# Optimization experiments

Measured on AMD Instinct MI355X. Metric: run time of the kernel, lower is better.

Reference implementation:

```python
import jax, jax.numpy as jnp
import numpy as np

N, E, D, T, R, H = 100000, 500000, 128, 3, 4, 8
DK = D // H
MAXLEN = 240
L = 2


def _rte_table():
    # Replicates RelTemporalEncoding sinusoidal table (note original precedence:
    # div_term = 1 / ((10000 ** arange(0, 2d, 2)) / d / 2); large exponents overflow
    # to inf in fp32 -> div entries become 0, matching torch behaviour).
    pos = jnp.arange(MAXLEN, dtype=jnp.float32)[:, None]            # [240, 1]
    ar = jnp.arange(0.0, 2 * D, 2.0, dtype=jnp.float32)             # [D]
    div = 1.0 / (jnp.power(jnp.float32(10000.0), ar) / D / 2.0)
    ang = pos * div                                                  # [240, D]
    s = np.float32(1.0 / np.sqrt(D))
    tab = jnp.zeros((MAXLEN, 2 * D), jnp.float32)
    tab = tab.at[:, 0::2].set(jnp.sin(ang) * s)
    tab = tab.at[:, 1::2].set(jnp.cos(ang) * s)
    return tab


def _typed_linear(x, W, b, types):
    # per-row type-specific affine: small fixed loop over node types
    out = jnp.zeros((x.shape[0], W.shape[-1]), x.dtype)
    for t in range(W.shape[0]):
        m = (types == t)[:, None].astype(x.dtype)
        out = out + m * (x @ W[t] + b[t])
    return out


def _typed_mm(x, W, types):
    out = jnp.zeros((x.shape[0], W.shape[-1]), x.dtype)
    for t in range(W.shape[0]):
        out = out + (types == t)[:, None].astype(x.dtype) * (x @ W[t])
    return out


def _hgt_layer(x, node_type, src, tgt, edge_type, edge_time, rte_tab,
               Wk, bk, Wq, bq, Wv, bv, Wa, ba, rel_pri, rel_att, rel_msg,
               skip, rte_w, rte_b):
    st = node_type[src]
    tt = node_type[tgt]
    # node-level typed projections (Q uses raw target feats; K/V bias+feat part)
    Qn = _typed_linear(x, Wq, bq, node_type)
    Kn = _typed_linear(x, Wk, bk, node_type)
    Vn = _typed_linear(x, Wv, bv, node_type)
    # per-edge temporal encoding added to source features before K/V linears;
    # linearity lets us add its typed projection (no double bias)
    rte = rte_tab[edge_time] @ rte_w + rte_b                         # [E, D]
    q = Qn[tgt].reshape(-1, H, DK)
    k = (Kn[src] + _typed_mm(rte, Wk, st)).reshape(-1, H, DK)
    v = (Vn[src] + _typed_mm(rte, Wv, st)).reshape(-1, H, DK)
    k2 = jnp.zeros_like(k)
    v2 = jnp.zeros_like(v)
    for r in range(R):  # small fixed relation loop, masked per-edge
        m = (edge_type == r)[:, None, None].astype(x.dtype)
        k2 = k2 + m * jnp.einsum('ehk,hkl->ehl', k, rel_att[r])
        v2 = v2 + m * jnp.einsum('ehk,hkl->ehl', v, rel_msg[r])
    pri = rel_pri[tt, edge_type, st]                                 # [E, H]
    score = (q * k2).sum(-1) * pri / np.float32(np.sqrt(DK))         # [E, H]
    # scatter-softmax over edges grouped by target node
    mx = jax.ops.segment_max(score, tgt, num_segments=N)
    ex = jnp.exp(score - mx[tgt])
    den = jax.ops.segment_sum(ex, tgt, num_segments=N)
    att = ex / den[tgt]
    msg = (v2 * att[:, :, None]).reshape(-1, D)
    aggr = jax.ops.segment_sum(msg, tgt, num_segments=N)             # [N, D]
    h = jax.nn.gelu(aggr, approximate=False)
    trans = _typed_linear(h, Wa, ba, node_type)
    alpha = jax.nn.sigmoid(skip)[node_type][:, None]
    return alpha * trans + (1.0 - alpha) * x


def setup_inputs() -> dict:
    key = jax.random.key(0)
    ks = jax.random.split(key, 20)
    s = np.float32(1.0 / np.sqrt(D))
    return {
        'node_feature': jax.random.normal(ks[0], (N, D), jnp.float32),
        'node_type': jax.random.randint(ks[1], (N,), 0, T, jnp.int32),
        'edge_index': jax.random.randint(ks[2], (2, E), 0, N, jnp.int32),
        'edge_type': jax.random.randint(ks[3], (E,), 0, R, jnp.int32),
        'edge_time': jax.random.randint(ks[4], (E,), 0, MAXLEN, jnp.int32),
        'adapt_w': jax.random.normal(ks[5], (T, D, D), jnp.float32) * s,
        'adapt_b': jax.random.normal(ks[6], (T, D), jnp.float32) * 0.01,
        'Wk': jax.random.normal(ks[7], (L, T, D, D), jnp.float32) * s,
        'bk': jax.random.normal(ks[8], (L, T, D), jnp.float32) * 0.01,
        'Wq': jax.random.normal(ks[9], (L, T, D, D), jnp.float32) * s,
        'bq': jax.random.normal(ks[10], (L, T, D), jnp.float32) * 0.01,
        'Wv': jax.random.normal(ks[11], (L, T, D, D), jnp.float32) * s,
        'bv': jax.random.normal(ks[12], (L, T, D), jnp.float32) * 0.01,
        'Wa': jax.random.normal(ks[13], (L, T, D, D), jnp.float32) * s,
        'ba': jax.random.normal(ks[14], (L, T, D), jnp.float32) * 0.01,
        'rel_pri': jnp.ones((L, T, R, T, H), jnp.float32),
        'rel_att': jax.random.normal(ks[15], (L, R, H, DK, DK), jnp.float32) * np.float32(1.0 / np.sqrt(DK)),
        'rel_msg': jax.random.normal(ks[16], (L, R, H, DK, DK), jnp.float32) * np.float32(1.0 / np.sqrt(DK)),
        'skip': jnp.ones((L, T), jnp.float32),
        'rte_w': jax.random.normal(ks[17], (L, 2 * D, D), jnp.float32) * np.float32(1.0 / np.sqrt(2 * D)),
        'rte_b': jax.random.normal(ks[18], (L, D), jnp.float32) * 0.01,
    }


def reference(node_feature, node_type, edge_index, edge_type, edge_time,
              adapt_w, adapt_b, Wk, bk, Wq, bq, Wv, bv, Wa, ba,
              rel_pri, rel_att, rel_msg, skip, rte_w, rte_b):
    rte_tab = _rte_table()
    src, tgt = edge_index[0], edge_index[1]
    # GNN input adaptation: typed linear + tanh (dropout = 0 / eval mode)
    x = jnp.tanh(_typed_linear(node_feature, adapt_w, adapt_b, node_type))
    for l in range(L):
        x = _hgt_layer(x, node_type, src, tgt, edge_type, edge_time, rte_tab,
                       Wk[l], bk[l], Wq[l], bq[l], Wv[l], bv[l], Wa[l], ba[l],
                       rel_pri[l], rel_att[l], rel_msg[l], skip[l],
                       rte_w[l], rte_b[l])
    return x
```

## Files before the change

kernel.cpp:

```cpp
#include <hip/hip_runtime.h>
#include <math.h>

#define NN 100000
#define EE 500000

__global__ void rte_tab_kernel(float* __restrict__ tab) {
    int p = blockIdx.x;
    int j = threadIdx.x;
    int m = j >> 1;
    float pf = (float)pow(10000.0, (double)(2 * m));
    float dv = 1.0f / (pf / 128.0f / 2.0f);
    float ang = (float)p * dv;
    const float s = 0.08838834764831845f;
    float v = (j & 1) ? (cosf(ang) * s) : (sinf(ang) * s);
    tab[p * 256 + j] = v;
}

__global__ void rte_proj_kernel(const float* __restrict__ tab,
                                const float* __restrict__ rte_w,
                                const float* __restrict__ rte_b,
                                float* __restrict__ proj) {
    __shared__ float row[256];
    int p = blockIdx.x;
    int c = threadIdx.x;
    for (int i = threadIdx.x; i < 256; i += 128) row[i] = tab[p * 256 + i];
    __syncthreads();
    float acc = rte_b[c];
    #pragma unroll 8
    for (int q = 0; q < 256; ++q) acc += row[q] * rte_w[q * 128 + c];
    proj[p * 128 + c] = acc;
}

__global__ void ktv_kernel(const float* __restrict__ proj,
                           const float* __restrict__ Wk,
                           const float* __restrict__ Wv,
                           float* __restrict__ ktv) {
    __shared__ float row[128];
    int b = blockIdx.x;
    int t = b / 240, p = b % 240;
    int c = threadIdx.x;
    row[c] = proj[p * 128 + c];
    __syncthreads();
    const float* wk = Wk + t * 16384 + c;
    const float* wv = Wv + t * 16384 + c;
    float ak = 0.f, av = 0.f;
    #pragma unroll 8
    for (int q = 0; q < 128; ++q) {
        float rv = row[q];
        ak += rv * wk[q * 128];
        av += rv * wv[q * 128];
    }
    ktv[(size_t)b * 256 + c] = ak;
    ktv[(size_t)b * 256 + 128 + c] = av;
}

__global__ void hist_kernel(const int* __restrict__ tgt, int* __restrict__ cnt) {
    int e = blockIdx.x * blockDim.x + threadIdx.x;
    if (e < EE) atomicAdd(&cnt[tgt[e]], 1);
}

__global__ void scan_kernel(const int* __restrict__ cnt, int* __restrict__ row_start) {
    __shared__ int sdata[1024];
    __shared__ int s_running;
    if (threadIdx.x == 0) s_running = 0;
    __syncthreads();
    for (int base = 0; base < NN; base += 1024) {
        int i = base + (int)threadIdx.x;
        int v = (i < NN) ? cnt[i] : 0;
        sdata[threadIdx.x] = v;
        __syncthreads();
        int acc = v;
        for (int off = 1; off < 1024; off <<= 1) {
            int t = (threadIdx.x >= (unsigned)off) ? sdata[threadIdx.x - off] : 0;
            __syncthreads();
            acc += t;
            sdata[threadIdx.x] = acc;
            __syncthreads();
        }
        int run = s_running;
        if (i < NN) row_start[i] = run + acc - v;
        __syncthreads();
        if (threadIdx.x == 1023) s_running = run + sdata[1023];
        __syncthreads();
    }
    if (threadIdx.x == 0) row_start[NN] = s_running;
}

__global__ void scatter_meta_kernel(const int* __restrict__ esrc,
                                    const int* __restrict__ etgt,
                                    const int* __restrict__ etype,
                                    const int* __restrict__ etime,
                                    const int* __restrict__ node_type,
                                    const int* __restrict__ row_start,
                                    int* __restrict__ fill,
                                    int4* __restrict__ meta) {
    int e = blockIdx.x * blockDim.x + threadIdx.x;
    if (e < EE) {
        int tgt = etgt[e];
        int src = esrc[e];
        int r = etype[e];
        int tm = etime[e];
        int st = node_type[src];
        int tt = node_type[tgt];
        int tb = st * 240 + tm;
        int pos = row_start[tgt] + atomicAdd(&fill[tgt], 1);
        meta[pos] = make_int4(src, (tb << 6) | (tt << 4) | (st << 2) | r, tgt, 0);
    }
}

__global__ void node_hist_kernel(const int* __restrict__ nt, int* __restrict__ tcnt) {
    __shared__ int lc[3];
    if (threadIdx.x < 3) lc[threadIdx.x] = 0;
    __syncthreads();
    int i = blockIdx.x * blockDim.x + threadIdx.x;
    if (i < NN) atomicAdd(&lc[nt[i]], 1);
    __syncthreads();
    if (threadIdx.x < 3) atomicAdd(&tcnt[threadIdx.x], lc[threadIdx.x]);
}

__global__ void node_scatter_kernel(const int* __restrict__ nt,
                                    const int* __restrict__ tcnt,
                                    int* __restrict__ fill3,
                                    int* __restrict__ order) {
    __shared__ int lc[3], lbase[3], lfill[3];
    if (threadIdx.x < 3) { lc[threadIdx.x] = 0; lfill[threadIdx.x] = 0; }
    __syncthreads();
    int i = blockIdx.x * blockDim.x + threadIdx.x;
    int t = -1;
    if (i < NN) { t = nt[i]; atomicAdd(&lc[t], 1); }
    __syncthreads();
    if (threadIdx.x < 3) lbase[threadIdx.x] = atomicAdd(&fill3[threadIdx.x], lc[threadIdx.x]);
    __syncthreads();
    if (i < NN) {
        int rank = atomicAdd(&lfill[t], 1);
        int tb = (t == 0) ? 0 : ((t == 1) ? tcnt[0] : tcnt[0] + tcnt[1]);
        order[tb + lbase[t] + rank] = i;
    }
}

template <int MODE>
__global__ __launch_bounds__(256) void typed_lin_kernel(
    const float* __restrict__ in, const int* __restrict__ nt,
    const int* __restrict__ order,
    const float* __restrict__ W, const float* __restrict__ b,
    const float* __restrict__ skip, float* __restrict__ out) {
    __shared__ float xs[32][128];
    __shared__ int rows[32];
    __shared__ int sty[32];
    int nb = blockIdx.x * 32;
    if (threadIdx.x < 32) {
        int r = order[nb + threadIdx.x];
        rows[threadIdx.x] = r;
        sty[threadIdx.x] = nt[r];
    }
    __syncthreads();
    for (int i = threadIdx.x; i < 1024; i += 256) {
        int nl = i >> 5, e4 = i & 31;
        *(float4*)&xs[nl][e4 * 4] = *(const float4*)(in + (size_t)rows[nl] * 128 + e4 * 4);
    }
    __syncthreads();
    int col = threadIdx.x & 127;
    int ng  = (threadIdx.x >> 7) * 16;
    int t0 = sty[ng];
    bool uni = true;
    #pragma unroll
    for (int ii = 1; ii < 16; ++ii) uni &= (sty[ng + ii] == t0);
    if (uni) {
        const float* w = W + t0 * 16384 + col;
        float bv = b[t0 * 128 + col];
        float alpha = (MODE == 1) ? (1.f / (1.f + __expf(-skip[t0]))) : 0.f;
        float acc[16];
        #pragma unroll
        for (int ii = 0; ii < 16; ++ii) acc[ii] = bv;
        for (int k0 = 0; k0 < 128; k0 += 4) {
            float w0 = w[(k0 + 0) * 128];
            float w1 = w[(k0 + 1) * 128];
            float w2 = w[(k0 + 2) * 128];
            float w3 = w[(k0 + 3) * 128];
            #pragma unroll
            for (int ii = 0; ii < 16; ++ii) {
                float4 xv = *(const float4*)&xs[ng + ii][k0];
                acc[ii] += xv.x * w0 + xv.y * w1 + xv.z * w2 + xv.w * w3;
            }
        }
        #pragma unroll
        for (int ii = 0; ii < 16; ++ii) {
            size_t gi = (size_t)rows[ng + ii] * 128 + col;
            if (MODE == 0) out[gi] = tanhf(acc[ii]);
            else           out[gi] = alpha * acc[ii] + (1.f - alpha) * out[gi];
        }
    } else {
        for (int ii = 0; ii < 16; ++ii) {
            int nl = ng + ii;
            int t = sty[nl];
            const float* w = W + t * 16384 + col;
            float acc = b[t * 128 + col];
            #pragma unroll 8
            for (int k = 0; k < 128; ++k) acc += xs[nl][k] * w[k * 128];
            size_t gi = (size_t)rows[nl] * 128 + col;
            if (MODE == 0) out[gi] = tanhf(acc);
            else {
                float alpha = 1.f / (1.f + __expf(-skip[t]));
                out[gi] = alpha * acc + (1.f - alpha) * out[gi];
            }
        }
    }
}

__global__ __launch_bounds__(256) void qkv_kernel(
    const float* __restrict__ x, const int* __restrict__ nt,
    const int* __restrict__ order,
    const float* __restrict__ Wq, const float* __restrict__ bq,
    const float* __restrict__ Wk, const float* __restrict__ bk,
    const float* __restrict__ Wv, const float* __restrict__ bv,
    float* __restrict__ Qn, float* __restrict__ KV) {
    __shared__ float xs[32][128];
    __shared__ int rows[32];
    __shared__ int sty[32];
    int nb = blockIdx.x * 32;
    if (threadIdx.x < 32) {
        int r = order[nb + threadIdx.x];
        rows[threadIdx.x] = r;
        sty[threadIdx.x] = nt[r];
    }
    __syncthreads();
    for (int i = threadIdx.x; i < 1024; i += 256) {
        int nl = i >> 5, e4 = i & 31;
        *(float4*)&xs[nl][e4 * 4] = *(const float4*)(x + (size_t)rows[nl] * 128 + e4 * 4);
    }
    __syncthreads();
    int col = threadIdx.x & 127;
    int ng  = (threadIdx.x >> 7) * 16;
    int t0 = sty[ng];
    bool uni = true;
    #pragma unroll
    for (int ii = 1; ii < 16; ++ii) uni &= (sty[ng + ii] == t0);
    if (uni) {
        const float* wq = Wq + t0 * 16384 + col;
        const float* wk = Wk + t0 * 16384 + col;
        const float* wv = Wv + t0 * 16384 + col;
        float bqv = bq[t0 * 128 + col];
        float bkv = bk[t0 * 128 + col];
        float bvv = bv[t0 * 128 + col];
        float aq[16], ak[16], av[16];
        #pragma unroll
        for (int ii = 0; ii < 16; ++ii) { aq[ii] = bqv; ak[ii] = bkv; av[ii] = bvv; }
        for (int k0 = 0; k0 < 128; k0 += 4) {
            float q0 = wq[(k0 + 0) * 128], q1 = wq[(k0 + 1) * 128];
            float q2 = wq[(k0 + 2) * 128], q3 = wq[(k0 + 3) * 128];
            float k0w = wk[(k0 + 0) * 128], k1w = wk[(k0 + 1) * 128];
            float k2w = wk[(k0 + 2) * 128], k3w = wk[(k0 + 3) * 128];
            float v0 = wv[(k0 + 0) * 128], v1 = wv[(k0 + 1) * 128];
            float v2 = wv[(k0 + 2) * 128], v3 = wv[(k0 + 3) * 128];
            #pragma unroll
            for (int ii = 0; ii < 16; ++ii) {
                float4 xv = *(const float4*)&xs[ng + ii][k0];
                aq[ii] += xv.x * q0 + xv.y * q1 + xv.z * q2 + xv.w * q3;
                ak[ii] += xv.x * k0w + xv.y * k1w + xv.z * k2w + xv.w * k3w;
                av[ii] += xv.x * v0 + xv.y * v1 + xv.z * v2 + xv.w * v3;
            }
        }
        #pragma unroll
        for (int ii = 0; ii < 16; ++ii) {
            size_t row = (size_t)rows[ng + ii];
            Qn[row * 128 + col] = aq[ii];
            KV[row * 256 + col] = ak[ii];
            KV[row * 256 + 128 + col] = av[ii];
        }
    } else {
        for (int ii = 0; ii < 16; ++ii) {
            int nl = ng + ii;
            int t = sty[nl];
            const float* wq = Wq + t * 16384 + col;
            const float* wk = Wk + t * 16384 + col;
            const float* wv = Wv + t * 16384 + col;
            float aq = bq[t * 128 + col];
            float ak = bk[t * 128 + col];
            float av = bv[t * 128 + col];
            #pragma unroll 4
            for (int k = 0; k < 128; ++k) {
                float xv = xs[nl][k];
                aq += xv * wq[k * 128];
                ak += xv * wk[k * 128];
                av += xv * wv[k * 128];
            }
            size_t row = (size_t)rows[nl];
            Qn[row * 128 + col] = aq;
            KV[row * 256 + col] = ak;
            KV[row * 256 + 128 + col] = av;
        }
    }
}

__global__ __launch_bounds__(256) void score2_kernel(
    const float* __restrict__ Qn, const float* __restrict__ KV,
    const float* __restrict__ ktv, const int4* __restrict__ meta,
    const int* __restrict__ node_type,
    const float* __restrict__ rel_pri, const float* __restrict__ rel_att,
    const int* __restrict__ row_start,
    float* __restrict__ p_out, float* __restrict__ inv_out) {
    __shared__ float qrow[4][128];
    __shared__ float qAs[4][512];
    int w = threadIdx.x >> 6;
    int lane = threadIdx.x & 63;
    int n = blockIdx.x * 4 + w;

    *(float2*)&qrow[w][lane * 2] = *(const float2*)(Qn + (size_t)n * 128 + lane * 2);
    __syncthreads();
    #pragma unroll
    for (int u = 0; u < 8; ++u) {
        int f = u * 64 + lane;
        int rem = f & 127;
        int hh = rem >> 4;
        const float4* A4 = (const float4*)(rel_att + (size_t)f * 16);
        float4 a0 = A4[0], a1 = A4[1], a2 = A4[2], a3 = A4[3];
        const float* qq = &qrow[w][hh * 16];
        float val = a0.x * qq[0] + a0.y * qq[1] + a0.z * qq[2] + a0.w * qq[3]
                  + a1.x * qq[4] + a1.y * qq[5] + a1.z * qq[6] + a1.w * qq[7]
                  + a2.x * qq[8] + a2.y * qq[9] + a2.z * qq[10] + a2.w * qq[11]
                  + a3.x * qq[12] + a3.y * qq[13] + a3.z * qq[14] + a3.w * qq[15];
        qAs[w][f] = val;
    }
    __syncthreads();

    int tt = node_type[n];
    int e_beg = row_start[n], e_end = row_start[n + 1];
    int j = lane >> 3, h = lane & 7;
    float ls = 0.f;
    for (int cb = e_beg; cb < e_end; cb += 8) {
        int ei = cb + j;
        bool valid = ei < e_end;
        int4 m = valid ? meta[ei] : make_int4(0, 0, 0, 0);
        int r = m.y & 3, st = (m.y >> 2) & 3, tb = m.y >> 6;
        const float4* kp = (const float4*)(KV + (size_t)m.x * 256 + h * 16);
        const float4* tp = (const float4*)(ktv + (size_t)tb * 256 + h * 16);
        float4 k0 = kp[0], k1 = kp[1], k2 = kp[2], k3 = kp[3];
        float4 t0 = tp[0], t1 = tp[1], t2 = tp[2], t3 = tp[3];
        const float* qa = &qAs[w][r * 128 + h * 16];
        float s = (k0.x + t0.x) * qa[0]  + (k0.y + t0.y) * qa[1]
                + (k0.z + t0.z) * qa[2]  + (k0.w + t0.w) * qa[3]
                + (k1.x + t1.x) * qa[4]  + (k1.y + t1.y) * qa[5]
                + (k1.z + t1.z) * qa[6]  + (k1.w + t1.w) * qa[7]
                + (k2.x + t2.x) * qa[8]  + (k2.y + t2.y) * qa[9]
                + (k2.z + t2.z) * qa[10] + (k2.w + t2.w) * qa[11]
                + (k3.x + t3.x) * qa[12] + (k3.y + t3.y) * qa[13]
                + (k3.z + t3.z) * qa[14] + (k3.w + t3.w) * qa[15];
        float pri = rel_pri[((tt * 4 + r) * 3 + st) * 8 + h];
        float p = valid ? __expf(s * pri * 0.25f) : 0.f;
        if (valid) p_out[(size_t)ei * 8 + h] = p;
        ls += p;
    }
    ls += __shfl_xor(ls, 8, 64);
    ls += __shfl_xor(ls, 16, 64);
    ls += __shfl_xor(ls, 32, 64);
    if (j == 0) inv_out[n * 8 + h] = (ls > 0.f) ? (1.f / ls) : 0.f;
}

__global__ __launch_bounds__(256) void aggr_kernel(
    const float* __restrict__ KV, const float* __restrict__ ktv,
    const int4* __restrict__ meta, const float* __restrict__ p,
    const float* __restrict__ inv, const int* __restrict__ row_start,
    const float* __restrict__ rel_msg, float* __restrict__ h_out) {
    __shared__ float accb[4][4][136];
    int w = threadIdx.x >> 6;
    int n = blockIdx.x * 4 + w;
    int lane = threadIdx.x & 63;
    int d0 = lane * 2;
    int h = lane >> 3;
    int cp = d0 & 15;
    int e_beg = row_start[n], e_end = row_start[n + 1];
    float2 a0 = {0.f, 0.f}, a1 = {0.f, 0.f}, a2 = {0.f, 0.f}, a3 = {0.f, 0.f};
    int rmask = 0;
    for (int cb = e_beg; cb < e_end; cb += 64) {
        int cdeg = min(64, e_end - cb);
        int4 mm = (cb + lane < e_end) ? meta[cb + lane] : make_int4(0, 0, 0, 0);
        int mx = mm.x, my = mm.y;
        #pragma unroll 4
        for (int i = 0; i < cdeg; ++i) {
            int src  = __shfl(mx, i, 64);
            int code = __shfl(my, i, 64);
            int r = code & 3;
            float pv = p[(size_t)(cb + i) * 8 + h];
            float2 v1 = *(const float2*)(KV + (size_t)src * 256 + 128 + d0);
            float2 v2 = *(const float2*)(ktv + (size_t)(code >> 6) * 256 + 128 + d0);
            float vx = pv * (v1.x + v2.x);
            float vy = pv * (v1.y + v2.y);
            rmask |= (1 << r);
            switch (r) {
                case 0: a0.x += vx; a0.y += vy; break;
                case 1: a1.x += vx; a1.y += vy; break;
                case 2: a2.x += vx; a2.y += vy; break;
                default: a3.x += vx; a3.y += vy; break;
            }
        }
    }
    int li = h * 17 + cp;
    accb[w][0][li] = a0.x; accb[w][0][li + 1] = a0.y;
    accb[w][1][li] = a1.x; accb[w][1][li + 1] = a1.y;
    accb[w][2][li] = a2.x; accb[w][2][li + 1] = a2.y;
    accb[w][3][li] = a3.x; accb[w][3][li + 1] = a3.y;
    __syncthreads();
    float o0 = 0.f, o1 = 0.f;
    const float* M = rel_msg + h * 256 + cp;
    #pragma unroll
    for (int r = 0; r < 4; ++r) {
        if (rmask & (1 << r)) {
            #pragma unroll
            for (int i = 0; i < 16; ++i) {
                float av = accb[w][r][h * 17 + i];
                float2 mm2 = *(const float2*)(M + r * 2048 + i * 16);
                o0 += av * mm2.x;
                o1 += av * mm2.y;
            }
        }
    }
    float iv = inv[n * 8 + h];
    o0 *= iv; o1 *= iv;
    o0 = 0.5f * o0 * (1.f + erff(o0 * 0.7071067811865475f));
    o1 = 0.5f * o1 * (1.f + erff(o1 * 0.7071067811865475f));
    *(float2*)(h_out + (size_t)n * 128 + d0) = make_float2(o0, o1);
}

extern "C" void kernel_launch(void* const* d_in, const int* in_sizes, int n_in,
                              void* d_out, int out_size, void* d_ws, size_t ws_size,
                              hipStream_t stream) {
    const float* node_feature = (const float*)d_in[0];
    const int*   node_type    = (const int*)d_in[1];
    const int*   edge_index   = (const int*)d_in[2];
    const int*   edge_type    = (const int*)d_in[3];
    const int*   edge_time    = (const int*)d_in[4];
    const float* adapt_w      = (const float*)d_in[5];
    const float* adapt_b      = (const float*)d_in[6];
    const float* Wk           = (const float*)d_in[7];
    const float* bk           = (const float*)d_in[8];
    const float* Wq           = (const float*)d_in[9];
    const float* bq           = (const float*)d_in[10];
    const float* Wv           = (const float*)d_in[11];
    const float* bv           = (const float*)d_in[12];
    const float* Wa           = (const float*)d_in[13];
    const float* ba           = (const float*)d_in[14];
    const float* rel_pri      = (const float*)d_in[15];
    const float* rel_att      = (const float*)d_in[16];
    const float* rel_msg      = (const float*)d_in[17];
    const float* skip         = (const float*)d_in[18];
    const float* rte_w        = (const float*)d_in[19];
    const float* rte_b        = (const float*)d_in[20];
    float* out = (float*)d_out;

    const size_t ND = (size_t)NN * 128;
    float* Qn     = (float*)d_ws;
    float* KV     = Qn + ND;
    float* rtab   = KV + 2 * ND;
    float* rproj  = rtab + 240 * 256;
    float* ktv    = rproj + 240 * 128;
    float* pbuf   = ktv + 720 * 256;
    float* invl   = pbuf + (size_t)EE * 8;
    int*   cnt    = (int*)(invl + (size_t)NN * 8);
    int*   fill   = cnt + NN;
    int*   row_st = fill + NN;
    int*   order  = row_st + NN + 4;
    int*   tcnt   = order + NN;
    int*   fill3  = tcnt + 4;
    int4*  meta   = (int4*)(fill3 + 4);

    const int* esrc = edge_index;
    const int* etgt = edge_index + EE;

    hipMemsetAsync(cnt, 0, 2 * NN * sizeof(int), stream);
    hipMemsetAsync(tcnt, 0, 8 * sizeof(int), stream);
    rte_tab_kernel<<<240, 256, 0, stream>>>(rtab);
    hist_kernel<<<(EE + 255) / 256, 256, 0, stream>>>(etgt, cnt);
    scan_kernel<<<1, 1024, 0, stream>>>(cnt, row_st);
    scatter_meta_kernel<<<(EE + 255) / 256, 256, 0, stream>>>(esrc, etgt, edge_type,
                                                              edge_time, node_type,
                                                              row_st, fill, meta);
    node_hist_kernel<<<(NN + 255) / 256, 256, 0, stream>>>(node_type, tcnt);
    node_scatter_kernel<<<(NN + 255) / 256, 256, 0, stream>>>(node_type, tcnt, fill3, order);

    typed_lin_kernel<0><<<NN / 32, 256, 0, stream>>>(node_feature, node_type, order,
                                                     adapt_w, adapt_b, nullptr, out);

    for (int l = 0; l < 2; ++l) {
        const float* Wk_l = Wk + l * 49152;  const float* bk_l = bk + l * 384;
        const float* Wq_l = Wq + l * 49152;  const float* bq_l = bq + l * 384;
        const float* Wv_l = Wv + l * 49152;  const float* bv_l = bv + l * 384;
        const float* Wa_l = Wa + l * 49152;  const float* ba_l = ba + l * 384;
        const float* pri_l = rel_pri + l * 288;
        const float* att_l = rel_att + l * 8192;
        const float* msg_l = rel_msg + l * 8192;
        const float* skip_l = skip + l * 3;
        const float* rte_w_l = rte_w + l * 32768;
        const float* rte_b_l = rte_b + l * 128;

        rte_proj_kernel<<<240, 128, 0, stream>>>(rtab, rte_w_l, rte_b_l, rproj);
        ktv_kernel<<<720, 128, 0, stream>>>(rproj, Wk_l, Wv_l, ktv);
        qkv_kernel<<<NN / 32, 256, 0, stream>>>(out, node_type, order, Wq_l, bq_l,
                                                Wk_l, bk_l, Wv_l, bv_l, Qn, KV);
        score2_kernel<<<NN / 4, 256, 0, stream>>>(Qn, KV, ktv, meta, node_type,
                                                  pri_l, att_l, row_st, pbuf, invl);
        aggr_kernel<<<NN / 4, 256, 0, stream>>>(KV, ktv, meta, pbuf, invl, row_st,
                                                msg_l, Qn );
        typed_lin_kernel<1><<<NN / 32, 256, 0, stream>>>(Qn, node_type, order, Wa_l, ba_l,
                                                         skip_l, out);
    }
}
```

Baseline: 1.864 ms.

## Fuse attention score and message aggregation into a single edge kernel

Merges the score kernel and the aggregation kernel into one edge_kernel. Per-edge softmax numerators now stay in per-warp shared scratch for each 64-edge chunk instead of going to a global E×8 buffer, and the normalisation sum is reduced in registers instead of going to a global inverse buffer. This removes one launch and the global write and re-read of the probability array, and meta is loaded once per chunk for both phases. In exchange, block-wide barriers are added inside the chunk loop, so every warp in a block iterates to the largest chunk count among its four nodes, which can leave warps idle when degrees are uneven.

```diff
diff --git a/kernel.cpp b/kernel.cpp
--- a/kernel.cpp
+++ b/kernel.cpp
@@ -292,21 +292,32 @@
     }
 }
 
-__global__ __launch_bounds__(256) void score2_kernel(
+__global__ __launch_bounds__(256) void edge_kernel(
     const float* __restrict__ Qn, const float* __restrict__ KV,
     const float* __restrict__ ktv, const int4* __restrict__ meta,
     const int* __restrict__ node_type,
     const float* __restrict__ rel_pri, const float* __restrict__ rel_att,
-    const int* __restrict__ row_start,
-    float* __restrict__ p_out, float* __restrict__ inv_out) {
-    __shared__ float qrow[4][128];
-    __shared__ float qAs[4][512];
+    const float* __restrict__ rel_msg, const int* __restrict__ row_start,
+    float* __restrict__ h_out) {
+    __shared__ float smem[4][1056];
+    __shared__ int chs[4];
     int w = threadIdx.x >> 6;
     int lane = threadIdx.x & 63;
     int n = blockIdx.x * 4 + w;
-
-    *(float2*)&qrow[w][lane * 2] = *(const float2*)(Qn + (size_t)n * 128 + lane * 2);
-    __syncthreads();
+    float* qAs_w   = smem[w];
+    float* scratch = smem[w] + 512;
+
+    int e_beg = row_start[n], e_end = row_start[n + 1];
+    int tt = node_type[n];
+    int4 mm0 = make_int4(0, 0, 0, 0);
+    if (e_beg + lane < e_end) mm0 = meta[e_beg + lane];
+
+    float2 q2 = *(const float2*)(Qn + (size_t)n * 128 + lane * 2);
+    *(float2*)&scratch[lane * 2] = q2;
+    if (lane == 0) chs[w] = (e_end - e_beg + 63) >> 6;
+    __syncthreads();
+    int nch = max(max(chs[0], chs[1]), max(chs[2], chs[3]));
+
     #pragma unroll
     for (int u = 0; u < 8; ++u) {
         int f = u * 64 + lane;
@@ -314,107 +325,110 @@
         int hh = rem >> 4;
         const float4* A4 = (const float4*)(rel_att + (size_t)f * 16);
         float4 a0 = A4[0], a1 = A4[1], a2 = A4[2], a3 = A4[3];
-        const float* qq = &qrow[w][hh * 16];
+        const float* qq = &scratch[hh * 16];
         float val = a0.x * qq[0] + a0.y * qq[1] + a0.z * qq[2] + a0.w * qq[3]
                   + a1.x * qq[4] + a1.y * qq[5] + a1.z * qq[6] + a1.w * qq[7]
                   + a2.x * qq[8] + a2.y * qq[9] + a2.z * qq[10] + a2.w * qq[11]
                   + a3.x * qq[12] + a3.y * qq[13] + a3.z * qq[14] + a3.w * qq[15];
-        qAs[w][f] = val;
-    }
-    __syncthreads();
-
-    int tt = node_type[n];
-    int e_beg = row_start[n], e_end = row_start[n + 1];
+        qAs_w[f] = val;
+    }
+    __syncthreads();
+
     int j = lane >> 3, h = lane & 7;
+    int h2 = lane >> 3, d0 = lane * 2;
+    int cp = d0 & 15;
     float ls = 0.f;
-    for (int cb = e_beg; cb < e_end; cb += 8) {
-        int ei = cb + j;
-        bool valid = ei < e_end;
-        int4 m = valid ? meta[ei] : make_int4(0, 0, 0, 0);
-        int r = m.y & 3, st = (m.y >> 2) & 3, tb = m.y >> 6;
-        const float4* kp = (const float4*)(KV + (size_t)m.x * 256 + h * 16);
-        const float4* tp = (const float4*)(ktv + (size_t)tb * 256 + h * 16);
-        float4 k0 = kp[0], k1 = kp[1], k2 = kp[2], k3 = kp[3];
-        float4 t0 = tp[0], t1 = tp[1], t2 = tp[2], t3 = tp[3];
-        const float* qa = &qAs[w][r * 128 + h * 16];
-        float s = (k0.x + t0.x) * qa[0]  + (k0.y + t0.y) * qa[1]
-                + (k0.z + t0.z) * qa[2]  + (k0.w + t0.w) * qa[3]
-                + (k1.x + t1.x) * qa[4]  + (k1.y + t1.y) * qa[5]
-                + (k1.z + t1.z) * qa[6]  + (k1.w + t1.w) * qa[7]
-                + (k2.x + t2.x) * qa[8]  + (k2.y + t2.y) * qa[9]
-                + (k2.z + t2.z) * qa[10] + (k2.w + t2.w) * qa[11]
-                + (k3.x + t3.x) * qa[12] + (k3.y + t3.y) * qa[13]
-                + (k3.z + t3.z) * qa[14] + (k3.w + t3.w) * qa[15];
-        float pri = rel_pri[((tt * 4 + r) * 3 + st) * 8 + h];
-        float p = valid ? __expf(s * pri * 0.25f) : 0.f;
-        if (valid) p_out[(size_t)ei * 8 + h] = p;
-        ls += p;
-    }
+    float2 a0v = {0.f, 0.f}, a1v = {0.f, 0.f}, a2v = {0.f, 0.f}, a3v = {0.f, 0.f};
+    int rmask = 0;
+
+    for (int c = 0; c < nch; ++c) {
+        int cb = e_beg + (c << 6);
+        bool active = cb < e_end;
+        int4 mm = mm0;
+        if (c > 0) {
+            mm = make_int4(0, 0, 0, 0);
+            if (active && (cb + lane) < e_end) mm = meta[cb + lane];
+        }
+        if (active) {
+            int nss = (min(64, e_end - cb) + 7) >> 3;
+            for (int ss = 0; ss < nss; ++ss) {
+                int icb = ss << 3;
+                int ei = cb + icb + j;
+                bool valid = ei < e_end;
+                int mxs = __shfl(mm.x, icb + j, 64);
+                int mys = __shfl(mm.y, icb + j, 64);
+                int r = mys & 3, st = (mys >> 2) & 3, tb = mys >> 6;
+                const float4* kp = (const float4*)(KV + (size_t)mxs * 256 + h * 16);
+                const float4* tp = (const float4*)(ktv + (size_t)tb * 256 + h * 16);
+                float4 k0 = kp[0], k1 = kp[1], k2 = kp[2], k3 = kp[3];
+                float4 t0 = tp[0], t1 = tp[1], t2 = tp[2], t3 = tp[3];
+                const float* qa = qAs_w + r * 128 + h * 16;
+                float s = (k0.x + t0.x) * qa[0]  + (k0.y + t0.y) * qa[1]
+                        + (k0.z + t0.z) * qa[2]  + (k0.w + t0.w) * qa[3]
+                        + (k1.x + t1.x) * qa[4]  + (k1.y + t1.y) * qa[5]
+                        + (k1.z + t1.z) * qa[6]  + (k1.w + t1.w) * qa[7]
+                        + (k2.x + t2.x) * qa[8]  + (k2.y + t2.y) * qa[9]
+                        + (k2.z + t2.z) * qa[10] + (k2.w + t2.w) * qa[11]
+                        + (k3.x + t3.x) * qa[12] + (k3.y + t3.y) * qa[13]
+                        + (k3.z + t3.z) * qa[14] + (k3.w + t3.w) * qa[15];
+                float pri = rel_pri[((tt * 4 + r) * 3 + st) * 8 + h];
+                float p = valid ? __expf(s * pri * 0.25f) : 0.f;
+                scratch[icb * 8 + lane] = p;
+                ls += p;
+            }
+        }
+        __syncthreads();
+        if (active) {
+            int cdeg = min(64, e_end - cb);
+            int mx = mm.x, my = mm.y;
+            #pragma unroll 4
+            for (int i = 0; i < cdeg; ++i) {
+                int src  = __shfl(mx, i, 64);
+                int code = __shfl(my, i, 64);
+                int r = code & 3;
+                float pv = scratch[i * 8 + h2];
+                float2 v1 = *(const float2*)(KV + (size_t)src * 256 + 128 + d0);
+                float2 v2 = *(const float2*)(ktv + (size_t)(code >> 6) * 256 + 128 + d0);
+                float vx = pv * (v1.x + v2.x);
+                float vy = pv * (v1.y + v2.y);
+                rmask |= (1 << r);
+                switch (r) {
+                    case 0: a0v.x += vx; a0v.y += vy; break;
+                    case 1: a1v.x += vx; a1v.y += vy; break;
+                    case 2: a2v.x += vx; a2v.y += vy; break;
+                    default: a3v.x += vx; a3v.y += vy; break;
+                }
+            }
+        }
+        __syncthreads();
+    }
+
     ls += __shfl_xor(ls, 8, 64);
     ls += __shfl_xor(ls, 16, 64);
     ls += __shfl_xor(ls, 32, 64);
-    if (j == 0) inv_out[n * 8 + h] = (ls > 0.f) ? (1.f / ls) : 0.f;
-}
-
-__global__ __launch_bounds__(256) void aggr_kernel(
-    const float* __restrict__ KV, const float* __restrict__ ktv,
-    const int4* __restrict__ meta, const float* __restrict__ p,
-    const float* __restrict__ inv, const int* __restrict__ row_start,
-    const float* __restrict__ rel_msg, float* __restrict__ h_out) {
-    __shared__ float accb[4][4][136];
-    int w = threadIdx.x >> 6;
-    int n = blockIdx.x * 4 + w;
-    int lane = threadIdx.x & 63;
-    int d0 = lane * 2;
-    int h = lane >> 3;
-    int cp = d0 & 15;
-    int e_beg = row_start[n], e_end = row_start[n + 1];
-    float2 a0 = {0.f, 0.f}, a1 = {0.f, 0.f}, a2 = {0.f, 0.f}, a3 = {0.f, 0.f};
-    int rmask = 0;
-    for (int cb = e_beg; cb < e_end; cb += 64) {
-        int cdeg = min(64, e_end - cb);
-        int4 mm = (cb + lane < e_end) ? meta[cb + lane] : make_int4(0, 0, 0, 0);
-        int mx = mm.x, my = mm.y;
-        #pragma unroll 4
-        for (int i = 0; i < cdeg; ++i) {
-            int src  = __shfl(mx, i, 64);
-            int code = __shfl(my, i, 64);
-            int r = code & 3;
-            float pv = p[(size_t)(cb + i) * 8 + h];
-            float2 v1 = *(const float2*)(KV + (size_t)src * 256 + 128 + d0);
-            float2 v2 = *(const float2*)(ktv + (size_t)(code >> 6) * 256 + 128 + d0);
-            float vx = pv * (v1.x + v2.x);
-            float vy = pv * (v1.y + v2.y);
-            rmask |= (1 << r);
-            switch (r) {
-                case 0: a0.x += vx; a0.y += vy; break;
-                case 1: a1.x += vx; a1.y += vy; break;
-                case 2: a2.x += vx; a2.y += vy; break;
-                default: a3.x += vx; a3.y += vy; break;
-            }
-        }
-    }
-    int li = h * 17 + cp;
-    accb[w][0][li] = a0.x; accb[w][0][li + 1] = a0.y;
-    accb[w][1][li] = a1.x; accb[w][1][li + 1] = a1.y;
-    accb[w][2][li] = a2.x; accb[w][2][li + 1] = a2.y;
-    accb[w][3][li] = a3.x; accb[w][3][li + 1] = a3.y;
+
+    int li = h2 * 17 + cp;
+    scratch[0 * 136 + li] = a0v.x; scratch[0 * 136 + li + 1] = a0v.y;
+    scratch[1 * 136 + li] = a1v.x; scratch[1 * 136 + li + 1] = a1v.y;
+    scratch[2 * 136 + li] = a2v.x; scratch[2 * 136 + li + 1] = a2v.y;
+    scratch[3 * 136 + li] = a3v.x; scratch[3 * 136 + li + 1] = a3v.y;
     __syncthreads();
     float o0 = 0.f, o1 = 0.f;
-    const float* M = rel_msg + h * 256 + cp;
+    const float* M = rel_msg + h2 * 256 + cp;
     #pragma unroll
     for (int r = 0; r < 4; ++r) {
         if (rmask & (1 << r)) {
             #pragma unroll
             for (int i = 0; i < 16; ++i) {
-                float av = accb[w][r][h * 17 + i];
+                float av = scratch[r * 136 + h2 * 17 + i];
                 float2 mm2 = *(const float2*)(M + r * 2048 + i * 16);
                 o0 += av * mm2.x;
                 o1 += av * mm2.y;
             }
         }
     }
-    float iv = inv[n * 8 + h];
+    float lst = __shfl(ls, h2, 64);
+    float iv = (lst > 0.f) ? (1.f / lst) : 0.f;
     o0 *= iv; o1 *= iv;
     o0 = 0.5f * o0 * (1.f + erff(o0 * 0.7071067811865475f));
     o1 = 0.5f * o1 * (1.f + erff(o1 * 0.7071067811865475f));
@@ -453,9 +467,7 @@
     float* rtab   = KV + 2 * ND;
     float* rproj  = rtab + 240 * 256;
     float* ktv    = rproj + 240 * 128;
-    float* pbuf   = ktv + 720 * 256;
-    float* invl   = pbuf + (size_t)EE * 8;
-    int*   cnt    = (int*)(invl + (size_t)NN * 8);
+    int*   cnt    = (int*)(ktv + 720 * 256);
     int*   fill   = cnt + NN;
     int*   row_st = fill + NN;
     int*   order  = row_st + NN + 4;
@@ -496,10 +508,9 @@
         ktv_kernel<<<720, 128, 0, stream>>>(rproj, Wk_l, Wv_l, ktv);
         qkv_kernel<<<NN / 32, 256, 0, stream>>>(out, node_type, order, Wq_l, bq_l,
                                                 Wk_l, bk_l, Wv_l, bv_l, Qn, KV);
-        score2_kernel<<<NN / 4, 256, 0, stream>>>(Qn, KV, ktv, meta, node_type,
-                                                  pri_l, att_l, row_st, pbuf, invl);
-        aggr_kernel<<<NN / 4, 256, 0, stream>>>(KV, ktv, meta, pbuf, invl, row_st,
-                                                msg_l, Qn );
+        edge_kernel<<<NN / 4, 256, 0, stream>>>(Qn, KV, ktv, meta, node_type,
+                                                pri_l, att_l, msg_l, row_st,
+                                                Qn );
         typed_lin_kernel<1><<<NN / 32, 256, 0, stream>>>(Qn, node_type, order, Wa_l, ba_l,
                                                          skip_l, out);
     }
```

Result: no change. 1.873 ms (+0.5%).
